# Performance work log

Measured on AMD Instinct MI355X. Metric: run time of the kernel, lower is better.

The kernel has to match this reference:

```python
import jax, jax.numpy as jnp
import numpy as np

N = 50000
E = 800000
H = 8
DH = 32  # hidden 256 / heads 8


def gat_layer(h, src, dst, W, a_src, a_dst, b):
    # h: [N, 256] -> per-head projected features [N, H, DH]
    hp = (h @ W).reshape(N, H, DH)
    # per-node attention logits for src/dst roles: [N, H]
    s_src = jnp.einsum('nhd,hd->nh', hp, a_src)
    s_dst = jnp.einsum('nhd,hd->nh', hp, a_dst)
    e = jax.nn.leaky_relu(s_src[src] + s_dst[dst], negative_slope=0.2)  # [Et, H]
    # segment softmax over incoming edges of each dst node
    m = jax.ops.segment_max(e, dst, num_segments=N)  # [N, H]
    ex = jnp.exp(e - m[dst])
    denom = jax.ops.segment_sum(ex, dst, num_segments=N)  # [N, H] (>0: self-loops)
    alpha = ex / denom[dst]  # [Et, H]
    out = jax.ops.segment_sum(alpha[:, :, None] * hp[src], dst, num_segments=N)
    return out.reshape(N, H * DH) + b


def han_forward(x, edges, proj_W, proj_b, gat_W, gat_asrc, gat_adst, gat_b,
                sem_W1, sem_b1, sem_W2, cls_W1, cls_b1, cls_W2, cls_b2):
    h0 = x @ proj_W + proj_b  # [N, 256]
    loop = jnp.arange(N, dtype=edges.dtype)
    embs = []
    for p in range(edges.shape[0]):  # 3 meta-paths (fixed, small)
        src = jnp.concatenate([edges[p, 0], loop])  # add self-loops (PyG default)
        dst = jnp.concatenate([edges[p, 1], loop])
        h = h0
        for l in range(2):  # 2 GAT layers per meta-path
            h = gat_layer(h, src, dst, gat_W[p, l], gat_asrc[p, l], gat_adst[p, l], gat_b[p, l])
            h = jax.nn.elu(h)  # dropout: eval-mode no-op
        embs.append(h)
    emb = jnp.stack(embs, axis=1)  # [N, P, 256]
    scores = (jnp.tanh(emb @ sem_W1 + sem_b1) @ sem_W2).squeeze(-1)  # [N, P]
    w = jax.nn.softmax(scores, axis=1)
    z = jnp.sum(emb * w[:, :, None], axis=1)  # [N, 256]
    hcls = jax.nn.relu(z @ cls_W1 + cls_b1)
    logits = hcls @ cls_W2 + cls_b2  # [N, 2]
    return logits


def setup_inputs() -> dict:
    key = jax.random.key(0)
    ks = jax.random.split(key, 16)
    s = 0.05
    return {
        'x': jax.random.normal(ks[0], (N, 128), jnp.float32),
        'edges': jax.random.randint(ks[1], (3, 2, E), 0, N, dtype=jnp.int32),
        'proj_W': jax.random.normal(ks[2], (128, 256), jnp.float32) * s,
        'proj_b': jnp.zeros((256,), jnp.float32),
        'gat_W': jax.random.normal(ks[3], (3, 2, 256, 256), jnp.float32) * s,
        'gat_asrc': jax.random.normal(ks[4], (3, 2, H, DH), jnp.float32) * s,
        'gat_adst': jax.random.normal(ks[5], (3, 2, H, DH), jnp.float32) * s,
        'gat_b': jnp.zeros((3, 2, 256), jnp.float32),
        'sem_W1': jax.random.normal(ks[6], (256, 128), jnp.float32) * s,
        'sem_b1': jnp.zeros((128,), jnp.float32),
        'sem_W2': jax.random.normal(ks[7], (128, 1), jnp.float32) * s,
        'cls_W1': jax.random.normal(ks[8], (256, 128), jnp.float32) * s,
        'cls_b1': jnp.zeros((128,), jnp.float32),
        'cls_W2': jax.random.normal(ks[9], (128, 2), jnp.float32) * s,
        'cls_b2': jnp.zeros((2,), jnp.float32),
    }


def reference(x, edges, proj_W, proj_b, gat_W, gat_asrc, gat_adst, gat_b,
              sem_W1, sem_b1, sem_W2, cls_W1, cls_b1, cls_W2, cls_b2):
    return han_forward(x, edges, proj_W, proj_b, gat_W, gat_asrc, gat_adst, gat_b,
                       sem_W1, sem_b1, sem_W2, cls_W1, cls_b1, cls_W2, cls_b2)
```

## Files before the change

### kernel.cpp

```cpp
#include <hip/hip_runtime.h>
#include <hip/hip_fp16.h>
#include <math.h>

#define N_NODES 50000
#define N_EDG   800000
#define NH      8
#define DH      32
#define HID     256
#define MAXD    64

typedef __attribute__((ext_vector_type(8))) short bf16x8;
typedef __attribute__((ext_vector_type(4))) float f32x4;

__device__ __forceinline__ unsigned short f2bf(float x) {
    unsigned u = __float_as_uint(x);
    u += 0x7FFF + ((u >> 16) & 1);
    return (unsigned short)(u >> 16);
}
__device__ __forceinline__ float bf2f(unsigned short h) {
    return __uint_as_float(((unsigned)h) << 16);
}
__device__ __forceinline__ void split8(const float4& a, const float4& b,
                                       uint4& hi, uint4& lo) {
    float v[8] = {a.x,a.y,a.z,a.w,b.x,b.y,b.z,b.w};
    unsigned short h[8], l[8];
    #pragma unroll
    for (int i = 0; i < 8; ++i) { h[i] = f2bf(v[i]); l[i] = f2bf(v[i] - bf2f(h[i])); }
    hi = make_uint4(h[0]|((unsigned)h[1]<<16), h[2]|((unsigned)h[3]<<16),
                    h[4]|((unsigned)h[5]<<16), h[6]|((unsigned)h[7]<<16));
    lo = make_uint4(l[0]|((unsigned)l[1]<<16), l[2]|((unsigned)l[3]<<16),
                    l[4]|((unsigned)l[5]<<16), l[6]|((unsigned)l[7]<<16));
}
__device__ __forceinline__ void h8_to_pair(uint4 r, uint4& hi, uint4& lo) {
    const __half2* hp = (const __half2*)&r;
    unsigned short h[8], l[8];
    #pragma unroll
    for (int i = 0; i < 4; ++i) {
        float2 f = __half22float2(hp[i]);
        h[2*i]   = f2bf(f.x); l[2*i]   = f2bf(f.x - bf2f(h[2*i]));
        h[2*i+1] = f2bf(f.y); l[2*i+1] = f2bf(f.y - bf2f(h[2*i+1]));
    }
    hi = make_uint4(h[0]|((unsigned)h[1]<<16), h[2]|((unsigned)h[3]<<16),
                    h[4]|((unsigned)h[5]<<16), h[6]|((unsigned)h[7]<<16));
    lo = make_uint4(l[0]|((unsigned)l[1]<<16), l[2]|((unsigned)l[3]<<16),
                    l[4]|((unsigned)l[5]<<16), l[6]|((unsigned)l[7]<<16));
}

__device__ __forceinline__ void fmix2(float& alo, float& ahi, unsigned rv, float w) {
    asm("v_fma_mix_f32 %0, %1, %2, %0 op_sel:[0,0,0] op_sel_hi:[1,0,0]"
        : "+v"(alo) : "v"(rv), "v"(w));
    asm("v_fma_mix_f32 %0, %1, %2, %0 op_sel:[1,0,0] op_sel_hi:[1,0,0]"
        : "+v"(ahi) : "v"(rv), "v"(w));
}

template<int NC, int ACT, int OUTMODE, int AMODE>
__global__ __launch_bounds__(256)
void mfma_gemm_k(const float* __restrict__ A32p, const __half* __restrict__ A16p,
                 int lda,
                 const unsigned short* __restrict__ WThi,
                 const unsigned short* __restrict__ WTlo,
                 const float* __restrict__ bias,
                 float* __restrict__ C, __half* __restrict__ Ch,
                 int ldc, int M, int K) {
    __shared__ unsigned short sAh[128*32], sAl[128*32], sBh[128*32], sBl[128*32];
    const int tid  = threadIdx.x;
    const int lane = tid & 63;
    const int w    = tid >> 6;
    const int wr   = w >> 1, wc = w & 1;
    const int r0   = blockIdx.x * 128;
    const int c0   = blockIdx.y * 128;
    const int l15  = lane & 15, q = lane >> 4;

    const int cl8   = (((lane & 3) ^ ((lane >> 4) & 3)) << 3);
    const int lrow  = w*32 + (lane >> 2);
    const int gbrow0 = c0 + lrow, gbrow1 = c0 + lrow + 16;
    const int lbase = w * 1024;
    const int ldst  = lbase + lane * 8;

    const int srow = tid >> 2, slot = tid & 3;
    const size_t ga0 = (size_t)min(r0 + srow,      M - 1) * lda + slot * 8;
    const size_t ga1 = (size_t)min(r0 + srow + 64, M - 1) * lda + slot * 8;
    const int lda0 = srow*32 + ((slot ^ ((srow >> 2) & 3)) << 3);
    const int lda1 = lda0 + 64*32;

    f32x4 acc[4][4];
    #pragma unroll
    for (int i = 0; i < 4; ++i)
        #pragma unroll
        for (int j = 0; j < 4; ++j) acc[i][j] = (f32x4){0.f, 0.f, 0.f, 0.f};

    const int swzF = (l15 >> 2) & 3;
    const int qs   = ((q ^ swzF) << 3);

    const int nsteps = K >> 5;
    for (int s = 0; s < nsteps; ++s) {
        const int kc = s << 5;
        __syncthreads();
        uint4 h0, l0, h1, l1;
        if constexpr (AMODE == 0) {
            float4 f0a = *(const float4*)&A32p[ga0 + kc];
            float4 f0b = *(const float4*)&A32p[ga0 + kc + 4];
            float4 f1a = *(const float4*)&A32p[ga1 + kc];
            float4 f1b = *(const float4*)&A32p[ga1 + kc + 4];
            split8(f0a, f0b, h0, l0);
            split8(f1a, f1b, h1, l1);
        } else {
            uint4 r0v = *(const uint4*)&A16p[ga0 + kc];
            uint4 r1v = *(const uint4*)&A16p[ga1 + kc];
            h8_to_pair(r0v, h0, l0);
            h8_to_pair(r1v, h1, l1);
        }
        *(uint4*)&sAh[lda0] = h0; *(uint4*)&sAl[lda0] = l0;
        *(uint4*)&sAh[lda1] = h1; *(uint4*)&sAl[lda1] = l1;
        *(uint4*)&sBh[ldst]       = *(const uint4*)&WThi[(size_t)gbrow0*K + kc + cl8];
        *(uint4*)&sBh[ldst + 512] = *(const uint4*)&WThi[(size_t)gbrow1*K + kc + cl8];
        *(uint4*)&sBl[ldst]       = *(const uint4*)&WTlo[(size_t)gbrow0*K + kc + cl8];
        *(uint4*)&sBl[ldst + 512] = *(const uint4*)&WTlo[(size_t)gbrow1*K + kc + cl8];
        __syncthreads();

        bf16x8 fAh[4], fAl[4];
        #pragma unroll
        for (int t = 0; t < 4; ++t) {
            int ra = (wr*64 + t*16 + l15) * 32 + qs;
            fAh[t] = *(const bf16x8*)&sAh[ra];
            fAl[t] = *(const bf16x8*)&sAl[ra];
        }
        #pragma unroll
        for (int nt = 0; nt < 4; ++nt) {
            int rb = (wc*64 + nt*16 + l15) * 32 + qs;
            bf16x8 fBh = *(const bf16x8*)&sBh[rb];
            bf16x8 fBl = *(const bf16x8*)&sBl[rb];
            #pragma unroll
            for (int mt = 0; mt < 4; ++mt) {
                acc[mt][nt] = __builtin_amdgcn_mfma_f32_16x16x32_bf16(fAh[mt], fBh, acc[mt][nt], 0, 0, 0);
                acc[mt][nt] = __builtin_amdgcn_mfma_f32_16x16x32_bf16(fAh[mt], fBl, acc[mt][nt], 0, 0, 0);
                acc[mt][nt] = __builtin_amdgcn_mfma_f32_16x16x32_bf16(fAl[mt], fBh, acc[mt][nt], 0, 0, 0);
            }
        }
    }
    #pragma unroll
    for (int mt = 0; mt < 4; ++mt)
        #pragma unroll
        for (int nt = 0; nt < 4; ++nt) {
            int col = c0 + wc*64 + nt*16 + l15;
            float bb = bias ? bias[col] : 0.f;
            #pragma unroll
            for (int r = 0; r < 4; ++r) {
                int grow = r0 + wr*64 + mt*16 + q*4 + r;
                if (grow < M) {
                    float v = acc[mt][nt][r] + bb;
                    if (ACT == 1) v = tanhf(v);
                    else if (ACT == 2) v = fmaxf(v, 0.f);
                    size_t o = (size_t)grow * ldc + col;
                    if (OUTMODE == 2) Ch[o] = __float2half(v);
                    else              C[o] = v;
                }
            }
        }
}

__global__ __launch_bounds__(256)
void mfma_gemm3_k(const __half* __restrict__ A16p, int aoffz, int lda,
                  const unsigned short* __restrict__ WT, int l,
                  __half* __restrict__ hp3, int M) {
    __shared__ unsigned short sAh[128*32], sAl[128*32], sBh[128*32], sBl[128*32];
    const int p = blockIdx.z;
    A16p += (size_t)p * aoffz;
    const unsigned short* WThi = WT + (size_t)(2*p + l) * 131072;
    const unsigned short* WTlo = WThi + 65536;
    __half* Ch = hp3 + (size_t)p * N_NODES * HID;
    const int K = HID;

    const int tid  = threadIdx.x;
    const int lane = tid & 63;
    const int w    = tid >> 6;
    const int wr   = w >> 1, wc = w & 1;
    const int r0   = blockIdx.x * 128;
    const int c0   = blockIdx.y * 128;
    const int l15  = lane & 15, q = lane >> 4;

    const int cl8   = (((lane & 3) ^ ((lane >> 4) & 3)) << 3);
    const int lrow  = w*32 + (lane >> 2);
    const int gbrow0 = c0 + lrow, gbrow1 = c0 + lrow + 16;
    const int lbase = w * 1024;
    const int ldst  = lbase + lane * 8;

    const int srow = tid >> 2, slot = tid & 3;
    const size_t ga0 = (size_t)min(r0 + srow,      M - 1) * lda + slot * 8;
    const size_t ga1 = (size_t)min(r0 + srow + 64, M - 1) * lda + slot * 8;
    const int lda0 = srow*32 + ((slot ^ ((srow >> 2) & 3)) << 3);
    const int lda1 = lda0 + 64*32;

    f32x4 acc[4][4];
    #pragma unroll
    for (int i = 0; i < 4; ++i)
        #pragma unroll
        for (int j = 0; j < 4; ++j) acc[i][j] = (f32x4){0.f, 0.f, 0.f, 0.f};

    const int swzF = (l15 >> 2) & 3;
    const int qs   = ((q ^ swzF) << 3);

    for (int s = 0; s < 8; ++s) {
        const int kc = s << 5;
        __syncthreads();
        uint4 r0v = *(const uint4*)&A16p[ga0 + kc];
        uint4 r1v = *(const uint4*)&A16p[ga1 + kc];
        uint4 h0, l0, h1, l1;
        h8_to_pair(r0v, h0, l0);
        h8_to_pair(r1v, h1, l1);
        *(uint4*)&sAh[lda0] = h0; *(uint4*)&sAl[lda0] = l0;
        *(uint4*)&sAh[lda1] = h1; *(uint4*)&sAl[lda1] = l1;
        *(uint4*)&sBh[ldst]       = *(const uint4*)&WThi[(size_t)gbrow0*K + kc + cl8];
        *(uint4*)&sBh[ldst + 512] = *(const uint4*)&WThi[(size_t)gbrow1*K + kc + cl8];
        *(uint4*)&sBl[ldst]       = *(const uint4*)&WTlo[(size_t)gbrow0*K + kc + cl8];
        *(uint4*)&sBl[ldst + 512] = *(const uint4*)&WTlo[(size_t)gbrow1*K + kc + cl8];
        __syncthreads();

        bf16x8 fAh[4], fAl[4];
        #pragma unroll
        for (int t = 0; t < 4; ++t) {
            int ra = (wr*64 + t*16 + l15) * 32 + qs;
            fAh[t] = *(const bf16x8*)&sAh[ra];
            fAl[t] = *(const bf16x8*)&sAl[ra];
        }
        #pragma unroll
        for (int nt = 0; nt < 4; ++nt) {
            int rb = (wc*64 + nt*16 + l15) * 32 + qs;
            bf16x8 fBh = *(const bf16x8*)&sBh[rb];
            bf16x8 fBl = *(const bf16x8*)&sBl[rb];
            #pragma unroll
            for (int mt = 0; mt < 4; ++mt) {
                acc[mt][nt] = __builtin_amdgcn_mfma_f32_16x16x32_bf16(fAh[mt], fBh, acc[mt][nt], 0, 0, 0);
                acc[mt][nt] = __builtin_amdgcn_mfma_f32_16x16x32_bf16(fAh[mt], fBl, acc[mt][nt], 0, 0, 0);
                acc[mt][nt] = __builtin_amdgcn_mfma_f32_16x16x32_bf16(fAl[mt], fBh, acc[mt][nt], 0, 0, 0);
            }
        }
    }
    #pragma unroll
    for (int mt = 0; mt < 4; ++mt)
        #pragma unroll
        for (int nt = 0; nt < 4; ++nt) {
            int col = c0 + wc*64 + nt*16 + l15;
            #pragma unroll
            for (int r = 0; r < 4; ++r) {
                int grow = r0 + wr*64 + mt*16 + q*4 + r;
                if (grow < M)
                    Ch[(size_t)grow * HID + col] = __float2half(acc[mt][nt][r]);
            }
        }
}

__global__ __launch_bounds__(256)
void cvtWall_k(const float* __restrict__ gatW, const float* __restrict__ projW,
               const float* __restrict__ semW1, const float* __restrict__ clsW1,
               unsigned short* __restrict__ WT) {
    int y = blockIdx.y;
    const float* W; int K, N;
    if (y < 6)       { W = gatW + (size_t)y * 65536; K = 256; N = 256; }
    else if (y == 6) { W = projW; K = 128; N = 256; }
    else if (y == 7) { W = semW1; K = 256; N = 128; }
    else             { W = clsW1; K = 256; N = 128; }
    int idx = blockIdx.x * 256 + threadIdx.x;
    if (idx >= K * N) return;
    unsigned short* hi = WT + (size_t)y * 131072;
    unsigned short* lo = hi + 65536;
    int k = idx / N, n = idx - k * N;
    float v = W[idx];
    unsigned short h = f2bf(v);
    hi[n * K + k] = h;
    lo[n * K + k] = f2bf(v - bf2f(h));
}

__global__ __launch_bounds__(256)
void attn_scores3_k(const __half* __restrict__ hp3,
                    const float* __restrict__ gatAs, const float* __restrict__ gatAd,
                    int l, float* __restrict__ ssrc3, float* __restrict__ sdst3) {
    int p = blockIdx.y;
    int gid = blockIdx.x * 256 + threadIdx.x;
    if (gid >= N_NODES * NH) return;
    int h = gid & 7;
    const __half2* hv = (const __half2*)(hp3 + (size_t)p * N_NODES * HID + (size_t)gid * DH);
    const float* a = gatAs + (2*p + l) * HID + h * DH;
    const float* d = gatAd + (2*p + l) * HID + h * DH;
    float ss = 0.f, sd = 0.f;
    #pragma unroll
    for (int j = 0; j < 8; ++j) {
        float4 av = ((const float4*)a)[j], dv = ((const float4*)d)[j];
        float2 f0 = __half22float2(hv[2*j]);
        float2 f1 = __half22float2(hv[2*j + 1]);
        ss += f0.x*av.x + f0.y*av.y + f1.x*av.z + f1.y*av.w;
        sd += f0.x*dv.x + f0.y*dv.y + f1.x*dv.z + f1.y*dv.w;
    }
    ssrc3[p * N_NODES * NH + gid] = ss;
    sdst3[p * N_NODES * NH + gid] = sd;
}

__global__ __launch_bounds__(256)
void zero_k(int* p, int n) { int i = blockIdx.x*256 + threadIdx.x; if (i < n) p[i] = 0; }

__global__ __launch_bounds__(256)
void fill1_k(const int* __restrict__ edges, int* __restrict__ cnt3,
             unsigned short* __restrict__ slots3) {
    int e = blockIdx.x*256 + threadIdx.x;
    if (e >= 3*N_EDG) return;
    int p = e / N_EDG, i = e - p * N_EDG;
    const int* src = edges + (size_t)p * 2 * N_EDG;
    const int* dst = src + N_EDG;
    int s = src[i], d = dst[i];
    s = min(max(s, 0), N_NODES - 1);
    d = min(max(d, 0), N_NODES - 1);
    int pos = atomicAdd(&cnt3[p * N_NODES + d], 1);
    if (pos < MAXD)
        slots3[((size_t)p * N_NODES + d) * MAXD + pos] = (unsigned short)s;
}

__global__ __launch_bounds__(256)
void agg3_k(const int* __restrict__ cnt3, const unsigned short* __restrict__ slots3,
            const float* __restrict__ ssrc3, const float* __restrict__ sdst3,
            const __half* __restrict__ hp3, const float* __restrict__ gatB, int l,
            __half* __restrict__ emb16) {
    const int p = blockIdx.y;
    int wid  = (blockIdx.x * blockDim.x + threadIdx.x) >> 6;
    int lane = threadIdx.x & 63;
    if (wid >= N_NODES) return;
    const int n = wid;
    const unsigned short* srcs = slots3 + ((size_t)p * N_NODES + n) * MAXD;
    const float* s_src = ssrc3 + p * N_NODES * NH;
    const float* s_dst = sdst3 + p * N_NODES * NH;
    const __half* hp = hp3 + (size_t)p * N_NODES * HID;
    const float* bias = gatB + (2*p + l) * HID;
    const int deg = min(cnt3[p * N_NODES + n], MAXD);

    const int sub = lane & 31, eo = lane >> 5;
    const int h2  = sub >> 2;
    const float sd2 = s_dst[n*NH + h2];
    const uint4* hp4 = (const uint4*)hp;
    float dn = 0.f;
    float a0=0.f,a1=0.f,a2=0.f,a3=0.f,a4=0.f,a5=0.f,a6=0.f,a7=0.f;

    int i = eo;
    for (; i + 2 < deg; i += 4) {
        const int s0 = srcs[i];
        const int s1 = srcs[i + 2];
        const float x0 = s_src[s0*NH + h2];
        const float x1 = s_src[s1*NH + h2];
        const uint4 r0 = hp4[s0*32 + sub];
        const uint4 r1 = hp4[s1*32 + sub];
        float e0 = x0 + sd2; e0 = e0 > 0.f ? e0 : 0.2f * e0;
        float e1 = x1 + sd2; e1 = e1 > 0.f ? e1 : 0.2f * e1;
        const float w0 = __expf(e0), w1 = __expf(e1);
        dn += w0; dn += w1;
        fmix2(a0, a1, r0.x, w0); fmix2(a2, a3, r0.y, w0);
        fmix2(a4, a5, r0.z, w0); fmix2(a6, a7, r0.w, w0);
        fmix2(a0, a1, r1.x, w1); fmix2(a2, a3, r1.y, w1);
        fmix2(a4, a5, r1.z, w1); fmix2(a6, a7, r1.w, w1);
    }
    if (i < deg) {
        const int s0 = srcs[i];
        const float x0 = s_src[s0*NH + h2];
        const uint4 r0 = hp4[s0*32 + sub];
        float e0 = x0 + sd2; e0 = e0 > 0.f ? e0 : 0.2f * e0;
        const float w0 = __expf(e0);
        dn += w0;
        fmix2(a0, a1, r0.x, w0); fmix2(a2, a3, r0.y, w0);
        fmix2(a4, a5, r0.z, w0); fmix2(a6, a7, r0.w, w0);
    }
    dn += __shfl_xor(dn, 32);
    a0 += __shfl_xor(a0, 32); a1 += __shfl_xor(a1, 32);
    a2 += __shfl_xor(a2, 32); a3 += __shfl_xor(a3, 32);
    a4 += __shfl_xor(a4, 32); a5 += __shfl_xor(a5, 32);
    a6 += __shfl_xor(a6, 32); a7 += __shfl_xor(a7, 32);
    if (lane < 32) {
        float evs = s_src[n*NH + h2] + sd2;
        evs = evs > 0.f ? evs : 0.2f * evs;
        float ws = __expf(evs);
        dn += ws;
        const uint4 rs = hp4[n*32 + sub];
        fmix2(a0, a1, rs.x, ws); fmix2(a2, a3, rs.y, ws);
        fmix2(a4, a5, rs.z, ws); fmix2(a6, a7, rs.w, ws);

        float rdn = 1.f / dn;
        float v[8] = {a0,a1,a2,a3,a4,a5,a6,a7};
        const float4 b0 = *(const float4*)&bias[sub*8];
        const float4 b1 = *(const float4*)&bias[sub*8 + 4];
        v[0]=v[0]*rdn+b0.x; v[1]=v[1]*rdn+b0.y; v[2]=v[2]*rdn+b0.z; v[3]=v[3]*rdn+b0.w;
        v[4]=v[4]*rdn+b1.x; v[5]=v[5]*rdn+b1.y; v[6]=v[6]*rdn+b1.z; v[7]=v[7]*rdn+b1.w;
        unsigned short hh[8];
        #pragma unroll
        for (int k = 0; k < 8; ++k) {
            float e = v[k] > 0.f ? v[k] : expm1f(v[k]);
            hh[k] = __half_as_ushort(__float2half(e));
        }
        size_t o = (size_t)n * 768 + p * HID + sub * 8;
        *(uint4*)&emb16[o] = make_uint4(hh[0]|((unsigned)hh[1]<<16), hh[2]|((unsigned)hh[3]<<16),
                                        hh[4]|((unsigned)hh[5]<<16), hh[6]|((unsigned)hh[7]<<16));
    }
}

__global__ __launch_bounds__(256)
void score_z_k(const float* t, const float* __restrict__ W2,
               const __half* __restrict__ emb16, float* z) {
    int wid  = (blockIdx.x * blockDim.x + threadIdx.x) >> 6;
    int lane = threadIdx.x & 63;
    if (wid >= N_NODES) return;
    const int n = wid;
    float sc[3];
    #pragma unroll
    for (int p = 0; p < 3; ++p) {
        const float* tr = t + (size_t)(n*3 + p) * 128;
        float part = tr[lane] * W2[lane] + tr[64 + lane] * W2[64 + lane];
        #pragma unroll
        for (int o = 1; o < 64; o <<= 1) part += __shfl_xor(part, o);
        sc[p] = part;
    }
    float m  = fmaxf(sc[0], fmaxf(sc[1], sc[2]));
    float e0 = __expf(sc[0]-m), e1 = __expf(sc[1]-m), e2 = __expf(sc[2]-m);
    float rs = 1.f / (e0 + e1 + e2);
    e0 *= rs; e1 *= rs; e2 *= rs;
    const __half* er = emb16 + (size_t)n * 768;
    for (int c = lane; c < 256; c += 64) {
        float v0 = __half2float(er[c]);
        float v1 = __half2float(er[256 + c]);
        float v2 = __half2float(er[512 + c]);
        z[(size_t)n*384 + c] = e0*v0 + e1*v1 + e2*v2;
    }
}

__global__ __launch_bounds__(256)
void logits_k(const float* __restrict__ hcls, const float* __restrict__ W2,
              const float* __restrict__ b2, float* __restrict__ out) {
    int gid = blockIdx.x*256 + threadIdx.x;
    if (gid >= N_NODES * 2) return;
    int n = gid >> 1, o = gid & 1;
    const float* hr = hcls + (size_t)n * 128;
    float a = b2[o];
    #pragma unroll 4
    for (int j = 0; j < 128; ++j) a += hr[j] * W2[j*2 + o];
    out[gid] = a;
}

extern "C" void kernel_launch(void* const* d_in, const int* in_sizes, int n_in,
                              void* d_out, int out_size, void* d_ws, size_t ws_size,
                              hipStream_t stream) {
    (void)in_sizes; (void)n_in; (void)out_size; (void)ws_size;
    const float* x     = (const float*)d_in[0];
    const int*   edges = (const int*)  d_in[1];
    const float* projW = (const float*)d_in[2];
    const float* projb = (const float*)d_in[3];
    const float* gatW  = (const float*)d_in[4];
    const float* gatAs = (const float*)d_in[5];
    const float* gatAd = (const float*)d_in[6];
    const float* gatB  = (const float*)d_in[7];
    const float* semW1 = (const float*)d_in[8];
    const float* semb1 = (const float*)d_in[9];
    const float* semW2 = (const float*)d_in[10];
    const float* clsW1 = (const float*)d_in[11];
    const float* clsb1 = (const float*)d_in[12];
    const float* clsW2 = (const float*)d_in[13];
    const float* clsb2 = (const float*)d_in[14];
    float* out = (float*)d_out;

    char* base = (char*)d_ws;
    const size_t PLANE = (size_t)N_NODES * HID * 2;
    __half* hp3   = (__half*)(base);
    __half* emb16 = (__half*)(base + 3*PLANE);
    __half* h016  = (__half*)(base + 6*PLANE);
    char* small = base + 7*PLANE;
    float* ssrc3 = (float*)small;
    float* sdst3 = ssrc3 + 3*(size_t)N_NODES*NH;
    int*   cnt3  = (int*)(sdst3 + 3*(size_t)N_NODES*NH);
    unsigned short* WT = (unsigned short*)(cnt3 + 3*N_NODES);
    unsigned short* slots3 = WT + 9*131072;
    float* tbuf = (float*)base;
    float* hcls = (float*)(base + 6*PLANE);

    dim3 blk(256);
    const int gx = (N_NODES + 127) / 128;

    cvtWall_k<<<dim3(256, 9), blk, 0, stream>>>(gatW, projW, semW1, clsW1, WT);
    zero_k  <<<(3*N_NODES+255)/256, blk, 0, stream>>>(cnt3, 3*N_NODES);
    fill1_k <<<(3*N_EDG+255)/256,   blk, 0, stream>>>(edges, cnt3, slots3);

    mfma_gemm_k<256,0,2,0><<<dim3(gx,2), blk, 0, stream>>>(
        x, nullptr, 128, WT + 6*131072, WT + 6*131072 + 65536, projb,
        nullptr, h016, 256, N_NODES, 128);

    for (int l = 0; l < 2; ++l) {
        if (l == 0)
            mfma_gemm3_k<<<dim3(gx,2,3), blk, 0, stream>>>(
                h016, 0, HID, WT, 0, hp3, N_NODES);
        else
            mfma_gemm3_k<<<dim3(gx,2,3), blk, 0, stream>>>(
                emb16, HID, 3*HID, WT, 1, hp3, N_NODES);
        attn_scores3_k<<<dim3((N_NODES*NH+255)/256, 3), blk, 0, stream>>>(
            hp3, gatAs, gatAd, l, ssrc3, sdst3);
        agg3_k<<<dim3((N_NODES*64)/256, 3), blk, 0, stream>>>(
            cnt3, slots3, ssrc3, sdst3, hp3, gatB, l, emb16);
    }

    mfma_gemm_k<128,1,0,1><<<dim3((150000+127)/128, 1), blk, 0, stream>>>(
        nullptr, emb16, 256, WT + 7*131072, WT + 7*131072 + 65536, semb1,
        tbuf, nullptr, 128, 150000, 256);
    score_z_k<<<(N_NODES*64)/256, blk, 0, stream>>>(tbuf, semW2, emb16, tbuf);
    mfma_gemm_k<128,2,0,0><<<dim3(gx, 1), blk, 0, stream>>>(
        tbuf, nullptr, 384, WT + 8*131072, WT + 8*131072 + 65536, clsb1,
        hcls, nullptr, 128, N_NODES, 256);
    logits_k<<<(N_NODES*2+255)/256, blk, 0, stream>>>(hcls, clsW2, clsb2, out);
}
```

Baseline: 1.049 ms.

## Use fast math intrinsics and unroll GAT edge aggregation loop by eight

Replaces tanhf in the GEMM epilogue with an exp-and-reciprocal formula, swaps divisions for the hardware v_rcp_f32 instruction, and replaces expm1f in ELU with __expf minus one. It also adds an 8-edge unrolled loop in the GAT aggregation kernel so more gathers are in flight per wave. The aim is to cut transcendental and division cost and raise memory-level parallelism. The trade is slightly lower accuracy near zero for ELU and more register pressure from the wider unroll.

```diff
diff --git a/kernel.cpp b/kernel.cpp
--- a/kernel.cpp
+++ b/kernel.cpp
@@ -19,6 +19,11 @@
 }
 __device__ __forceinline__ float bf2f(unsigned short h) {
     return __uint_as_float(((unsigned)h) << 16);
+}
+__device__ __forceinline__ float fastrcp(float x) {
+    float r;
+    asm("v_rcp_f32 %0, %1" : "=v"(r) : "v"(x));
+    return r;
 }
 __device__ __forceinline__ void split8(const float4& a, const float4& b,
                                        uint4& hi, uint4& lo) {
@@ -149,8 +154,10 @@
                 int grow = r0 + wr*64 + mt*16 + q*4 + r;
                 if (grow < M) {
                     float v = acc[mt][nt][r] + bb;
-                    if (ACT == 1) v = tanhf(v);
-                    else if (ACT == 2) v = fmaxf(v, 0.f);
+                    if (ACT == 1) {
+                        float t = __expf(2.f * v);
+                        v = 1.f - 2.f * fastrcp(1.f + t);
+                    } else if (ACT == 2) v = fmaxf(v, 0.f);
                     size_t o = (size_t)grow * ldc + col;
                     if (OUTMODE == 2) Ch[o] = __float2half(v);
                     else              C[o] = v;
@@ -339,6 +346,35 @@
     float a0=0.f,a1=0.f,a2=0.f,a3=0.f,a4=0.f,a5=0.f,a6=0.f,a7=0.f;
 
     int i = eo;
+    for (; i + 6 < deg; i += 8) {
+        const int s0 = srcs[i];
+        const int s1 = srcs[i + 2];
+        const int s2 = srcs[i + 4];
+        const int s3 = srcs[i + 6];
+        const float x0 = s_src[s0*NH + h2];
+        const float x1 = s_src[s1*NH + h2];
+        const float x2 = s_src[s2*NH + h2];
+        const float x3 = s_src[s3*NH + h2];
+        const uint4 r0 = hp4[s0*32 + sub];
+        const uint4 r1 = hp4[s1*32 + sub];
+        const uint4 r2 = hp4[s2*32 + sub];
+        const uint4 r3 = hp4[s3*32 + sub];
+        float e0 = x0 + sd2; e0 = e0 > 0.f ? e0 : 0.2f * e0;
+        float e1 = x1 + sd2; e1 = e1 > 0.f ? e1 : 0.2f * e1;
+        float e2 = x2 + sd2; e2 = e2 > 0.f ? e2 : 0.2f * e2;
+        float e3 = x3 + sd2; e3 = e3 > 0.f ? e3 : 0.2f * e3;
+        const float w0 = __expf(e0), w1 = __expf(e1);
+        const float w2 = __expf(e2), w3 = __expf(e3);
+        dn += w0; dn += w1; dn += w2; dn += w3;
+        fmix2(a0, a1, r0.x, w0); fmix2(a2, a3, r0.y, w0);
+        fmix2(a4, a5, r0.z, w0); fmix2(a6, a7, r0.w, w0);
+        fmix2(a0, a1, r1.x, w1); fmix2(a2, a3, r1.y, w1);
+        fmix2(a4, a5, r1.z, w1); fmix2(a6, a7, r1.w, w1);
+        fmix2(a0, a1, r2.x, w2); fmix2(a2, a3, r2.y, w2);
+        fmix2(a4, a5, r2.z, w2); fmix2(a6, a7, r2.w, w2);
+        fmix2(a0, a1, r3.x, w3); fmix2(a2, a3, r3.y, w3);
+        fmix2(a4, a5, r3.z, w3); fmix2(a6, a7, r3.w, w3);
+    }
     for (; i + 2 < deg; i += 4) {
         const int s0 = srcs[i];
         const int s1 = srcs[i + 2];
@@ -379,7 +415,7 @@
         fmix2(a0, a1, rs.x, ws); fmix2(a2, a3, rs.y, ws);
         fmix2(a4, a5, rs.z, ws); fmix2(a6, a7, rs.w, ws);
 
-        float rdn = 1.f / dn;
+        float rdn = fastrcp(dn);
         float v[8] = {a0,a1,a2,a3,a4,a5,a6,a7};
         const float4 b0 = *(const float4*)&bias[sub*8];
         const float4 b1 = *(const float4*)&bias[sub*8 + 4];
@@ -388,7 +424,7 @@
         unsigned short hh[8];
         #pragma unroll
         for (int k = 0; k < 8; ++k) {
-            float e = v[k] > 0.f ? v[k] : expm1f(v[k]);
+            float e = v[k] > 0.f ? v[k] : (__expf(v[k]) - 1.f);
             hh[k] = __half_as_ushort(__float2half(e));
         }
         size_t o = (size_t)n * 768 + p * HID + sub * 8;
@@ -415,7 +451,7 @@
     }
     float m  = fmaxf(sc[0], fmaxf(sc[1], sc[2]));
     float e0 = __expf(sc[0]-m), e1 = __expf(sc[1]-m), e2 = __expf(sc[2]-m);
-    float rs = 1.f / (e0 + e1 + e2);
+    float rs = fastrcp(e0 + e1 + e2);
     e0 *= rs; e1 *= rs; e2 *= rs;
     const __half* er = emb16 + (size_t)n * 768;
     for (int c = lane; c < 256; c += 64) {
```

After: 1.053 ms. No clear change (+0.4%).
